# Kernel optimization log

Measured on AMD Instinct MI355X. Metric: run time of the kernel, lower is better.

The kernel has to match this reference:

```python
import jax, jax.numpy as jnp
import numpy as np

N = 100000   # nodes
R = 8        # relations
E = 800000   # edges per relation
D = 128      # in_feat == out_feat
B = 4        # num bases
L = 2        # ngnn layers


def setup_inputs() -> dict:
    key = jax.random.key(0)
    ks = jax.random.split(key, 8)
    x = jax.random.normal(ks[0], (N, D), dtype=jnp.float32)
    edge_src = jax.random.randint(ks[1], (R, E), 0, N, dtype=jnp.int64)
    edge_dst = jax.random.randint(ks[2], (R, E), 0, N, dtype=jnp.int64)
    scale = 1.0 / np.sqrt(D)
    w_comp = jax.random.normal(ks[3], (R, B), dtype=jnp.float32) * 0.3
    bases = jax.random.normal(ks[4], (B, D, D), dtype=jnp.float32) * scale
    loop_weight = jax.random.normal(ks[5], (D, D), dtype=jnp.float32) * scale
    h_bias = jnp.zeros((D,), dtype=jnp.float32)
    ngnn_w = jax.random.normal(ks[6], (L, D, D), dtype=jnp.float32) * scale
    return {"x": x, "edge_src": edge_src, "edge_dst": edge_dst,
            "w_comp": w_comp, "bases": bases, "loop_weight": loop_weight,
            "h_bias": h_bias, "ngnn_w": ngnn_w}


def reference(x, edge_src, edge_dst, w_comp, bases, loop_weight, h_bias, ngnn_w):
    # basis-decomposed per-relation weights: [R, D, D]
    weight = jnp.einsum('rb,bio->rio', w_comp, bases)
    h = jnp.zeros((N, D), dtype=x.dtype)
    # per-relation GraphConv, norm='right' (mean over in-degree, clamp min 1),
    # in_feat == out_feat so DGL aggregates first then applies weight;
    # HeteroGraphConv sums relation outputs for the shared dst type.
    for r in range(R):
        src, dst = edge_src[r], edge_dst[r]
        msg = jax.ops.segment_sum(x[src], dst, num_segments=N)           # [N, D]
        deg = jax.ops.segment_sum(jnp.ones((E,), x.dtype), dst, num_segments=N)
        agg = msg / jnp.maximum(deg, 1.0)[:, None]
        h = h + agg @ weight[r]
    # self loop + bias + activation
    h = jax.nn.relu(h + x @ loop_weight + h_bias)
    # NGNN MLP (dropout is identity in eval)
    for l in range(ngnn_w.shape[0]):
        h = jax.nn.relu(h @ ngnn_w[l])
    return h
```

## Files before the change

kernel.cpp:

```cpp
#include <hip/hip_runtime.h>
#include <hip/hip_bf16.h>

#define N_NODES 100000
#define R_REL   8
#define E_EDGES 800000
#define D_FEAT  128
#define B_BASES 4
#define RN      (R_REL * N_NODES)
#define RE      (R_REL * E_EDGES)

#define NBKT    784
#define BKT_CAP 9216
#define P1_TPB  256
#define P1_EPT  32
#define P1_CHUNK (P1_TPB * P1_EPT)
#define P1_NWG  ((RE + P1_CHUNK - 1) / P1_CHUNK)

#define SUB_PER_BKT 4
#define SGRID   (NBKT * SUB_PER_BKT)
#define SUBCAP  2816

typedef __attribute__((ext_vector_type(8))) short short8;
typedef __attribute__((ext_vector_type(4))) float floatx4;

__global__ __launch_bounds__(1024) void init_cursor_kernel(int* __restrict__ gcursor) {
    int t = threadIdx.x;
    if (t < NBKT) gcursor[t] = t * BKT_CAP;
}

__global__ __launch_bounds__(256) void xcvt_kernel(
    const float* __restrict__ x, uint* __restrict__ xb) {
    int i = blockIdx.x * 256 + threadIdx.x;
    if (i >= N_NODES * 64) return;
    float2 v = *(const float2*)(x + 2 * (size_t)i);
    __hip_bfloat162 h = __float22bfloat162_rn(v);
    xb[i] = *(uint*)&h;
}

__global__ __launch_bounds__(256) void wcvt_kernel(
    const float* __restrict__ bases, const float* __restrict__ loopw,
    unsigned short* __restrict__ wT) {
    int idx = blockIdx.x * 256 + threadIdx.x;
    if (idx >= 128 * 640) return;
    int n = idx / 640, k = idx % 640;
    float v = (k < 512) ? bases[(size_t)k * 128 + n] : loopw[(size_t)(k - 512) * 128 + n];
    __hip_bfloat16 h = __float2bfloat16(v);
    wT[idx] = *(unsigned short*)&h;
}

__global__ __launch_bounds__(256) void wcvt2_kernel(
    const float* __restrict__ ngnn_w, unsigned short* __restrict__ wT2) {
    int idx = blockIdx.x * 256 + threadIdx.x;
    if (idx >= 2 * 128 * 128) return;
    int l = idx >> 14, rem = idx & 16383;
    int n = rem >> 7, k = rem & 127;
    float v = ngnn_w[(size_t)l * 16384 + (size_t)k * 128 + n];
    __hip_bfloat16 h = __float2bfloat16(v);
    wT2[idx] = *(unsigned short*)&h;
}

__global__ __launch_bounds__(256) void p1_kernel(
    const int* __restrict__ src, const int* __restrict__ dst,
    int* __restrict__ gcursor, int* __restrict__ ebuf2) {
    __shared__ int hist[NBKT];
    __shared__ int cnt2[NBKT];
    __shared__ int basebkt[NBKT];
    __shared__ int lofs[NBKT];
    __shared__ int aux[256];
    __shared__ int recs[P1_CHUNK];
    __shared__ unsigned short bb[P1_CHUNK];
    int t = threadIdx.x;
    for (int i = t; i < NBKT; i += 256) { hist[i] = 0; cnt2[i] = 0; }
    __syncthreads();

    int e0 = blockIdx.x * P1_CHUNK;
    int rec[P1_EPT];
    int bkt[P1_EPT];
#pragma unroll
    for (int i = 0; i < P1_EPT; ++i) {
        int e = e0 + i * P1_TPB + t;
        if (e < RE) {
            int d = dst[e];
            int s = src[e];
            int r = e / E_EDGES;
            bkt[i] = d >> 7;
            rec[i] = s | ((d & 127) << 17) | (r << 24);
            atomicAdd(&hist[bkt[i]], 1);
        } else bkt[i] = -1;
    }
    __syncthreads();

    int k0 = t * 4;
    int c0 = (k0 + 0 < NBKT) ? hist[k0 + 0] : 0;
    int c1 = (k0 + 1 < NBKT) ? hist[k0 + 1] : 0;
    int c2 = (k0 + 2 < NBKT) ? hist[k0 + 2] : 0;
    int c3 = (k0 + 3 < NBKT) ? hist[k0 + 3] : 0;
    int s1 = c0 + c1, s2 = s1 + c2, s3 = s2 + c3;
    aux[t] = s3;
    __syncthreads();
    int vv = s3;
    for (int off = 1; off < 256; off <<= 1) {
        int yv = (t >= off) ? aux[t - off] : 0;
        __syncthreads();
        vv += yv;
        aux[t] = vv;
        __syncthreads();
    }
    int total = aux[255];
    int texcl = vv - s3;
    if (k0 + 0 < NBKT) lofs[k0 + 0] = texcl;
    if (k0 + 1 < NBKT) lofs[k0 + 1] = texcl + c0;
    if (k0 + 2 < NBKT) lofs[k0 + 2] = texcl + s1;
    if (k0 + 3 < NBKT) lofs[k0 + 3] = texcl + s2;
    __syncthreads();
    for (int i = t; i < NBKT; i += 256) {
        int hv = hist[i];
        basebkt[i] = (hv > 0) ? atomicAdd(&gcursor[i], hv) : 0;
    }
    __syncthreads();

#pragma unroll
    for (int i = 0; i < P1_EPT; ++i) {
        if (bkt[i] >= 0) {
            int p = lofs[bkt[i]] + atomicAdd(&cnt2[bkt[i]], 1);
            recs[p] = rec[i];
            bb[p] = (unsigned short)bkt[i];
        }
    }
    __syncthreads();

    for (int i = t; i < total; i += 256) {
        int b = bb[i];
        int p2 = basebkt[b] + (i - lofs[b]);
        if (p2 < (b + 1) * BKT_CAP) ebuf2[p2] = recs[i];
    }
}

template <bool XB>
__global__ __launch_bounds__(512, 8) void agg3_kernel(
    const float* __restrict__ x,
    const uint*  __restrict__ xb,
    const int*   __restrict__ gcursor,
    const int*   __restrict__ ebuf2,
    const float* __restrict__ w_comp,
    __hip_bfloat162* __restrict__ y) {
    __shared__ int raw[SUBCAP];
    __shared__ int sorted[SUBCAP];
    __shared__ int cursors[256];
    __shared__ int segbeg[256];
    __shared__ int nraw;
    const int t = threadIdx.x;
    const int bucket = blockIdx.x % NBKT;
    const int sub    = blockIdx.x / NBKT;

    int cnt = gcursor[bucket] - bucket * BKT_CAP;
    if (cnt > BKT_CAP) cnt = BKT_CAP;
    const int* brec = ebuf2 + (size_t)bucket * BKT_CAP;
    if (t < 256) cursors[t] = 0;
    if (t == 0) nraw = 0;
    __syncthreads();

    const int lane = t & 63;
    const unsigned long long lmask = (1ull << lane) - 1ull;

    for (int i0 = 0; i0 < cnt; i0 += 512) {
        int i = i0 + t;
        int rec = (i < cnt) ? brec[i] : 0;
        bool match = (i < cnt) && ((((rec >> 17) & 127) >> 5) == sub);
        unsigned long long mask = __ballot(match);
        int base = 0;
        if (lane == 0) base = atomicAdd(&nraw, (int)__popcll(mask));
        base = __shfl(base, 0);
        if (match) {
            int p = base + (int)__popcll(mask & lmask);
            if (p < SUBCAP) {
                raw[p] = rec;
                int key = ((rec >> 17) & 31) * 8 + ((rec >> 24) & 7);
                atomicAdd(&cursors[key], 1);
            }
        }
    }
    __syncthreads();
    int n = nraw; if (n > SUBCAP) n = SUBCAP;

    int deg = (t < 256) ? cursors[t] : 0;
    int* aux = sorted;
    aux[t] = deg;
    __syncthreads();
    int vv = deg;
    for (int off = 1; off < 256; off <<= 1) {
        int yv = (t >= off && t < 256) ? aux[t - off] : 0;
        __syncthreads();
        vv += yv;
        aux[t] = vv;
        __syncthreads();
    }
    if (t < 256) {
        cursors[t] = vv - deg;
        segbeg[t]  = vv - deg;
    }
    __syncthreads();

    for (int i = t; i < n; i += 512) {
        int rec = raw[i];
        int key = ((rec >> 17) & 31) * 8 + ((rec >> 24) & 7);
        int pos = atomicAdd(&cursors[key], 1);
        sorted[pos] = rec & 0x1FFFF;
    }
    __syncthreads();

    const int wid = t >> 6;
    const float* xp  = x + 2 * lane;
    const uint*  xbp = xb + lane;
    for (int nn = 0; nn < 4; ++nn) {
        int nl = wid * 4 + nn;
        int node = bucket * 128 + sub * 32 + nl;
        int key0 = nl * 8;
        float2 acc[B_BASES];
#pragma unroll
        for (int b = 0; b < B_BASES; ++b) acc[b] = make_float2(0.f, 0.f);
#pragma unroll
        for (int r = 0; r < R_REL; ++r) {
            int b0 = segbeg[key0 + r];
            int e0 = cursors[key0 + r];
            int d = e0 - b0;
            float inv = 1.0f / (float)(d > 1 ? d : 1);
            float ax = 0.f, ay = 0.f;
            int i = b0;
            for (; i + 3 < e0; i += 4) {
                int s0 = sorted[i], s1 = sorted[i + 1], s2 = sorted[i + 2], s3 = sorted[i + 3];
                if (XB) {
                    uint u0 = xbp[(size_t)s0 * 64];
                    uint u1 = xbp[(size_t)s1 * 64];
                    uint u2 = xbp[(size_t)s2 * 64];
                    uint u3 = xbp[(size_t)s3 * 64];
                    ax += (__uint_as_float(u0 << 16) + __uint_as_float(u1 << 16))
                        + (__uint_as_float(u2 << 16) + __uint_as_float(u3 << 16));
                    ay += (__uint_as_float(u0 & 0xFFFF0000u) + __uint_as_float(u1 & 0xFFFF0000u))
                        + (__uint_as_float(u2 & 0xFFFF0000u) + __uint_as_float(u3 & 0xFFFF0000u));
                } else {
                    float2 a = *(const float2*)(xp + (size_t)s0 * D_FEAT);
                    float2 b = *(const float2*)(xp + (size_t)s1 * D_FEAT);
                    float2 cc = *(const float2*)(xp + (size_t)s2 * D_FEAT);
                    float2 d2 = *(const float2*)(xp + (size_t)s3 * D_FEAT);
                    ax += (a.x + b.x) + (cc.x + d2.x);
                    ay += (a.y + b.y) + (cc.y + d2.y);
                }
            }
            for (; i < e0; ++i) {
                int s = sorted[i];
                if (XB) {
                    uint u = xbp[(size_t)s * 64];
                    ax += __uint_as_float(u << 16);
                    ay += __uint_as_float(u & 0xFFFF0000u);
                } else {
                    float2 a = *(const float2*)(xp + (size_t)s * D_FEAT);
                    ax += a.x; ay += a.y;
                }
            }
#pragma unroll
            for (int b = 0; b < B_BASES; ++b) {
                float coef = w_comp[r * B_BASES + b] * inv;
                acc[b].x = fmaf(coef, ax, acc[b].x);
                acc[b].y = fmaf(coef, ay, acc[b].y);
            }
        }
        if (node < N_NODES) {
#pragma unroll
            for (int b = 0; b < B_BASES; ++b)
                y[(size_t)node * 256 + b * 64 + lane] = __float22bfloat162_rn(acc[b]);
        }
    }
}

__global__ __launch_bounds__(256) void gemm_big_mfma(
    const short* __restrict__ y,
    const float* __restrict__ x,
    const unsigned short* __restrict__ wT,
    const float* __restrict__ bias,
    unsigned short* __restrict__ hb1) {
    const int wave = threadIdx.x >> 6;
    const int lane = threadIdx.x & 63;
    const int quad = lane >> 4;
    const int l16  = lane & 15;
    const int row0 = blockIdx.x * 64 + wave * 16;
    int arow = row0 + l16;
    if (arow >= N_NODES) arow = N_NODES - 1;

    floatx4 acc[8];
#pragma unroll
    for (int nt = 0; nt < 8; ++nt) acc[nt] = (floatx4){0.f, 0.f, 0.f, 0.f};

    const short* yrow = y + (size_t)arow * 512;
    const float* xrow = x + (size_t)arow * 128;
    const int koff = quad * 8;

    for (int ks = 0; ks < 16; ++ks) {
        int k0 = ks * 32 + koff;
        short8 a = *(const short8*)(yrow + k0);
#pragma unroll
        for (int nt = 0; nt < 8; ++nt) {
            int n = nt * 16 + l16;
            short8 b = *(const short8*)((const short*)wT + (size_t)n * 640 + k0);
            acc[nt] = __builtin_amdgcn_mfma_f32_16x16x32_bf16(a, b, acc[nt], 0, 0, 0);
        }
    }
#pragma unroll
    for (int ks = 0; ks < 4; ++ks) {
        int k0 = ks * 32 + koff;
        float4 fa = *(const float4*)(xrow + k0);
        float4 fb = *(const float4*)(xrow + k0 + 4);
        union { short8 s; uint u[4]; } ua;
        __hip_bfloat162 h0 = __float22bfloat162_rn(make_float2(fa.x, fa.y));
        __hip_bfloat162 h1 = __float22bfloat162_rn(make_float2(fa.z, fa.w));
        __hip_bfloat162 h2 = __float22bfloat162_rn(make_float2(fb.x, fb.y));
        __hip_bfloat162 h3 = __float22bfloat162_rn(make_float2(fb.z, fb.w));
        ua.u[0] = *(uint*)&h0; ua.u[1] = *(uint*)&h1;
        ua.u[2] = *(uint*)&h2; ua.u[3] = *(uint*)&h3;
#pragma unroll
        for (int nt = 0; nt < 8; ++nt) {
            int n = nt * 16 + l16;
            short8 b = *(const short8*)((const short*)wT + (size_t)n * 640 + 512 + k0);
            acc[nt] = __builtin_amdgcn_mfma_f32_16x16x32_bf16(ua.s, b, acc[nt], 0, 0, 0);
        }
    }

#pragma unroll
    for (int nt = 0; nt < 8; ++nt) {
        int n = nt * 16 + l16;
        float bs = bias[n];
#pragma unroll
        for (int i = 0; i < 4; ++i) {
            int m = row0 + quad * 4 + i;
            if (m < N_NODES) {
                float v = fmaxf(acc[nt][i] + bs, 0.f);
                __hip_bfloat16 h = __float2bfloat16(v);
                hb1[(size_t)m * D_FEAT + n] = *(unsigned short*)&h;
            }
        }
    }
}

template <bool OUT_BF16>
__global__ __launch_bounds__(256) void ngnn_mfma(
    const short* __restrict__ A,
    const unsigned short* __restrict__ wTl,
    void* __restrict__ C) {
    const int wave = threadIdx.x >> 6;
    const int lane = threadIdx.x & 63;
    const int quad = lane >> 4;
    const int l16  = lane & 15;
    const int row0 = blockIdx.x * 64 + wave * 16;
    int arow = row0 + l16;
    if (arow >= N_NODES) arow = N_NODES - 1;

    floatx4 acc[8];
#pragma unroll
    for (int nt = 0; nt < 8; ++nt) acc[nt] = (floatx4){0.f, 0.f, 0.f, 0.f};

    const short* ar = A + (size_t)arow * 128;
    const int koff = quad * 8;
#pragma unroll
    for (int ks = 0; ks < 4; ++ks) {
        int k0 = ks * 32 + koff;
        short8 a = *(const short8*)(ar + k0);
#pragma unroll
        for (int nt = 0; nt < 8; ++nt) {
            int n = nt * 16 + l16;
            short8 b = *(const short8*)((const short*)wTl + (size_t)n * 128 + k0);
            acc[nt] = __builtin_amdgcn_mfma_f32_16x16x32_bf16(a, b, acc[nt], 0, 0, 0);
        }
    }

#pragma unroll
    for (int nt = 0; nt < 8; ++nt) {
        int n = nt * 16 + l16;
#pragma unroll
        for (int i = 0; i < 4; ++i) {
            int m = row0 + quad * 4 + i;
            if (m < N_NODES) {
                float v = fmaxf(acc[nt][i], 0.f);
                if (OUT_BF16) {
                    __hip_bfloat16 h = __float2bfloat16(v);
                    ((unsigned short*)C)[(size_t)m * D_FEAT + n] = *(unsigned short*)&h;
                } else {
                    ((float*)C)[(size_t)m * D_FEAT + n] = v;
                }
            }
        }
    }
}

extern "C" void kernel_launch(void* const* d_in, const int* in_sizes, int n_in,
                              void* d_out, int out_size, void* d_ws, size_t ws_size,
                              hipStream_t stream) {
    const float* x           = (const float*)d_in[0];
    const int*   edge_src    = (const int*)d_in[1];
    const int*   edge_dst    = (const int*)d_in[2];
    const float* w_comp      = (const float*)d_in[3];
    const float* bases       = (const float*)d_in[4];
    const float* loop_weight = (const float*)d_in[5];
    const float* h_bias      = (const float*)d_in[6];
    const float* ngnn_w      = (const float*)d_in[7];
    float* out = (float*)d_out;

    char* ws = (char*)d_ws;
    size_t off = 0;
    __hip_bfloat162* y = (__hip_bfloat162*)(ws + off);
    off += (size_t)N_NODES * 512 * 2;
    int* ebuf2 = (int*)(ws + off);
    unsigned short* hb1 = (unsigned short*)(ws + off);
    off += (size_t)NBKT * BKT_CAP * 4;
    int* gcursor = (int*)(ws + off);
    off += 4096;
    unsigned short* wT = (unsigned short*)(ws + off);
    off += (size_t)128 * 640 * 2;
    unsigned short* wT2 = (unsigned short*)(ws + off);
    off += (size_t)2 * 128 * 128 * 2;
    uint* xb = (uint*)(ws + off);
    size_t xb_bytes = (size_t)N_NODES * 64 * 4;
    const bool use_bf16_x = (ws_size >= off + xb_bytes);
    unsigned short* hb2 = use_bf16_x ? (unsigned short*)xb : (unsigned short*)y;

    const int GEMM_GRID = (N_NODES + 63) / 64;

    wcvt_kernel<<<(128 * 640 + 255) / 256, 256, 0, stream>>>(bases, loop_weight, wT);
    wcvt2_kernel<<<(2 * 128 * 128 + 255) / 256, 256, 0, stream>>>(ngnn_w, wT2);
    if (use_bf16_x)
        xcvt_kernel<<<(N_NODES * 64 + 255) / 256, 256, 0, stream>>>(x, xb);

    init_cursor_kernel<<<1, 1024, 0, stream>>>(gcursor);
    p1_kernel<<<P1_NWG, P1_TPB, 0, stream>>>(edge_src, edge_dst, gcursor, ebuf2);

    if (use_bf16_x)
        agg3_kernel<true><<<SGRID, 512, 0, stream>>>(x, xb, gcursor, ebuf2, w_comp, y);
    else
        agg3_kernel<false><<<SGRID, 512, 0, stream>>>(x, nullptr, gcursor, ebuf2, w_comp, y);

    gemm_big_mfma<<<GEMM_GRID, 256, 0, stream>>>(
        (const short*)y, x, wT, h_bias, hb1);

    ngnn_mfma<true><<<GEMM_GRID, 256, 0, stream>>>(
        (const short*)hb1, wT2, (void*)hb2);
    ngnn_mfma<false><<<GEMM_GRID, 256, 0, stream>>>(
        (const short*)hb2, wT2 + 128 * 128, (void*)out);
}
```

Measured before the change: 701.2 us.

## Gather bf16 rows with 16-byte loads over four edges per wave

In the bf16 path of the aggregation kernel, each wave now splits into four 16-lane groups. Each group processes a different edge, and each lane loads a uint4 covering 8 features instead of one uint. Partial sums are combined with cross-lane shuffles before the bf16 store. The intent is fewer, wider gather instructions and more memory-level parallelism per wave, at the cost of more registers, extra shuffle reductions and masked tail handling. The block-to-bucket mapping also changes so that the four subblocks of a bucket are adjacent, and output stores become nontemporal.

```diff
diff --git a/kernel.cpp b/kernel.cpp
--- a/kernel.cpp
+++ b/kernel.cpp
@@ -135,6 +135,13 @@
         if (p2 < (b + 1) * BKT_CAP) ebuf2[p2] = recs[i];
     }
 }
+
+#define ACC4(u) do { \
+    ax0 += __uint_as_float((u).x << 16); ay0 += __uint_as_float((u).x & 0xFFFF0000u); \
+    ax1 += __uint_as_float((u).y << 16); ay1 += __uint_as_float((u).y & 0xFFFF0000u); \
+    ax2 += __uint_as_float((u).z << 16); ay2 += __uint_as_float((u).z & 0xFFFF0000u); \
+    ax3 += __uint_as_float((u).w << 16); ay3 += __uint_as_float((u).w & 0xFFFF0000u); \
+} while (0)
 
 template <bool XB>
 __global__ __launch_bounds__(512, 8) void agg3_kernel(
@@ -150,8 +157,8 @@
     __shared__ int segbeg[256];
     __shared__ int nraw;
     const int t = threadIdx.x;
-    const int bucket = blockIdx.x % NBKT;
-    const int sub    = blockIdx.x / NBKT;
+    const int bucket = blockIdx.x >> 2;
+    const int sub    = blockIdx.x & 3;
 
     int cnt = gcursor[bucket] - bucket * BKT_CAP;
     if (cnt > BKT_CAP) cnt = BKT_CAP;
@@ -210,35 +217,99 @@
     __syncthreads();
 
     const int wid = t >> 6;
-    const float* xp  = x + 2 * lane;
-    const uint*  xbp = xb + lane;
-    for (int nn = 0; nn < 4; ++nn) {
-        int nl = wid * 4 + nn;
-        int node = bucket * 128 + sub * 32 + nl;
-        int key0 = nl * 8;
-        float2 acc[B_BASES];
-#pragma unroll
-        for (int b = 0; b < B_BASES; ++b) acc[b] = make_float2(0.f, 0.f);
-#pragma unroll
-        for (int r = 0; r < R_REL; ++r) {
-            int b0 = segbeg[key0 + r];
-            int e0 = cursors[key0 + r];
-            int d = e0 - b0;
-            float inv = 1.0f / (float)(d > 1 ? d : 1);
-            float ax = 0.f, ay = 0.f;
-            int i = b0;
-            for (; i + 3 < e0; i += 4) {
-                int s0 = sorted[i], s1 = sorted[i + 1], s2 = sorted[i + 2], s3 = sorted[i + 3];
-                if (XB) {
-                    uint u0 = xbp[(size_t)s0 * 64];
-                    uint u1 = xbp[(size_t)s1 * 64];
-                    uint u2 = xbp[(size_t)s2 * 64];
-                    uint u3 = xbp[(size_t)s3 * 64];
-                    ax += (__uint_as_float(u0 << 16) + __uint_as_float(u1 << 16))
-                        + (__uint_as_float(u2 << 16) + __uint_as_float(u3 << 16));
-                    ay += (__uint_as_float(u0 & 0xFFFF0000u) + __uint_as_float(u1 & 0xFFFF0000u))
-                        + (__uint_as_float(u2 & 0xFFFF0000u) + __uint_as_float(u3 & 0xFFFF0000u));
-                } else {
+    if (XB) {
+        const int q  = lane & 15;
+        const int eg = lane >> 4;
+        const uint* xbq = xb + 4 * q;
+        for (int nn = 0; nn < 4; ++nn) {
+            int nl = wid * 4 + nn;
+            int node = bucket * 128 + sub * 32 + nl;
+            int key0 = nl * 8;
+            float2 a0[B_BASES], a1[B_BASES], a2[B_BASES], a3[B_BASES];
+#pragma unroll
+            for (int b = 0; b < B_BASES; ++b) {
+                a0[b] = make_float2(0.f, 0.f); a1[b] = make_float2(0.f, 0.f);
+                a2[b] = make_float2(0.f, 0.f); a3[b] = make_float2(0.f, 0.f);
+            }
+#pragma unroll
+            for (int r = 0; r < R_REL; ++r) {
+                int b0 = segbeg[key0 + r];
+                int e0 = cursors[key0 + r];
+                int len = e0 - b0;
+                float inv = 1.0f / (float)(len > 1 ? len : 1);
+                float ax0 = 0.f, ay0 = 0.f, ax1 = 0.f, ay1 = 0.f;
+                float ax2 = 0.f, ay2 = 0.f, ax3 = 0.f, ay3 = 0.f;
+                int it = 0;
+                for (; it + 8 <= len; it += 8) {
+                    int sA = sorted[b0 + it + eg];
+                    int sB = sorted[b0 + it + 4 + eg];
+                    uint4 uA = *(const uint4*)(xbq + (size_t)sA * 64);
+                    uint4 uB = *(const uint4*)(xbq + (size_t)sB * 64);
+                    ACC4(uA); ACC4(uB);
+                }
+                if (it + 4 <= len) {
+                    int sA = sorted[b0 + it + eg];
+                    uint4 uA = *(const uint4*)(xbq + (size_t)sA * 64);
+                    ACC4(uA);
+                    it += 4;
+                }
+                int rem = len - it;
+                if (rem > 0) {
+                    int idx = b0 + it + eg;
+                    int s = sorted[idx < e0 ? idx : e0 - 1];
+                    uint4 u = *(const uint4*)(xbq + (size_t)s * 64);
+                    if (eg >= rem) { u.x = 0u; u.y = 0u; u.z = 0u; u.w = 0u; }
+                    ACC4(u);
+                }
+#pragma unroll
+                for (int b = 0; b < B_BASES; ++b) {
+                    float c = w_comp[r * B_BASES + b] * inv;
+                    a0[b].x = fmaf(c, ax0, a0[b].x); a0[b].y = fmaf(c, ay0, a0[b].y);
+                    a1[b].x = fmaf(c, ax1, a1[b].x); a1[b].y = fmaf(c, ay1, a1[b].y);
+                    a2[b].x = fmaf(c, ax2, a2[b].x); a2[b].y = fmaf(c, ay2, a2[b].y);
+                    a3[b].x = fmaf(c, ax3, a3[b].x); a3[b].y = fmaf(c, ay3, a3[b].y);
+                }
+            }
+            if (node < N_NODES) {
+                uint* yrow = (uint*)(y + (size_t)node * 256);
+#pragma unroll
+                for (int b = 0; b < B_BASES; ++b) {
+                    float v0x = a0[b].x, v0y = a0[b].y, v1x = a1[b].x, v1y = a1[b].y;
+                    float v2x = a2[b].x, v2y = a2[b].y, v3x = a3[b].x, v3y = a3[b].y;
+                    v0x += __shfl_xor(v0x, 16); v0x += __shfl_xor(v0x, 32);
+                    v0y += __shfl_xor(v0y, 16); v0y += __shfl_xor(v0y, 32);
+                    v1x += __shfl_xor(v1x, 16); v1x += __shfl_xor(v1x, 32);
+                    v1y += __shfl_xor(v1y, 16); v1y += __shfl_xor(v1y, 32);
+                    v2x += __shfl_xor(v2x, 16); v2x += __shfl_xor(v2x, 32);
+                    v2y += __shfl_xor(v2y, 16); v2y += __shfl_xor(v2y, 32);
+                    v3x += __shfl_xor(v3x, 16); v3x += __shfl_xor(v3x, 32);
+                    v3y += __shfl_xor(v3y, 16); v3y += __shfl_xor(v3y, 32);
+                    float sx = (eg == 0) ? v0x : (eg == 1) ? v1x : (eg == 2) ? v2x : v3x;
+                    float sy = (eg == 0) ? v0y : (eg == 1) ? v1y : (eg == 2) ? v2y : v3y;
+                    __hip_bfloat162 h = __float22bfloat162_rn(make_float2(sx, sy));
+                    __builtin_nontemporal_store(*(uint*)&h, yrow + b * 64 + 4 * q + eg);
+                }
+            }
+        }
+    } else {
+        const float* xp = x + 2 * lane;
+        for (int nn = 0; nn < 4; ++nn) {
+            int nl = wid * 4 + nn;
+            int node = bucket * 128 + sub * 32 + nl;
+            int key0 = nl * 8;
+            float2 acc[B_BASES];
+#pragma unroll
+            for (int b = 0; b < B_BASES; ++b) acc[b] = make_float2(0.f, 0.f);
+#pragma unroll
+            for (int r = 0; r < R_REL; ++r) {
+                int b0 = segbeg[key0 + r];
+                int e0 = cursors[key0 + r];
+                int d = e0 - b0;
+                float inv = 1.0f / (float)(d > 1 ? d : 1);
+                float ax = 0.f, ay = 0.f;
+                int i = b0;
+                for (; i + 3 < e0; i += 4) {
+                    int s0 = sorted[i], s1 = sorted[i + 1], s2 = sorted[i + 2], s3 = sorted[i + 3];
                     float2 a = *(const float2*)(xp + (size_t)s0 * D_FEAT);
                     float2 b = *(const float2*)(xp + (size_t)s1 * D_FEAT);
                     float2 cc = *(const float2*)(xp + (size_t)s2 * D_FEAT);
@@ -246,29 +317,26 @@
                     ax += (a.x + b.x) + (cc.x + d2.x);
                     ay += (a.y + b.y) + (cc.y + d2.y);
                 }
-            }
-            for (; i < e0; ++i) {
-                int s = sorted[i];
-                if (XB) {
-                    uint u = xbp[(size_t)s * 64];
-                    ax += __uint_as_float(u << 16);
-                    ay += __uint_as_float(u & 0xFFFF0000u);
-                } else {
+                for (; i < e0; ++i) {
+                    int s = sorted[i];
                     float2 a = *(const float2*)(xp + (size_t)s * D_FEAT);
                     ax += a.x; ay += a.y;
                 }
-            }
-#pragma unroll
-            for (int b = 0; b < B_BASES; ++b) {
-                float coef = w_comp[r * B_BASES + b] * inv;
-                acc[b].x = fmaf(coef, ax, acc[b].x);
-                acc[b].y = fmaf(coef, ay, acc[b].y);
-            }
-        }
-        if (node < N_NODES) {
-#pragma unroll
-            for (int b = 0; b < B_BASES; ++b)
-                y[(size_t)node * 256 + b * 64 + lane] = __float22bfloat162_rn(acc[b]);
+#pragma unroll
+                for (int b = 0; b < B_BASES; ++b) {
+                    float coef = w_comp[r * B_BASES + b] * inv;
+                    acc[b].x = fmaf(coef, ax, acc[b].x);
+                    acc[b].y = fmaf(coef, ay, acc[b].y);
+                }
+            }
+            if (node < N_NODES) {
+                uint* yrow = (uint*)(y + (size_t)node * 256);
+#pragma unroll
+                for (int b = 0; b < B_BASES; ++b) {
+                    __hip_bfloat162 h = __float22bfloat162_rn(acc[b]);
+                    __builtin_nontemporal_store(*(uint*)&h, yrow + b * 64 + lane);
+                }
+            }
         }
     }
 }
```

Measured after the change: 1.614 ms. 2.3x slower.

## Fuse big GEMM and both NGNN layers into one kernel via LDS tiles

Applied to the files above, without the earlier changes.

Merges the main projection GEMM and the two NGNN MLP layers into one kernel. Each wave stages its 16x128 bf16 intermediate activations in a padded shared-memory tile instead of writing them to global memory. This removes two kernel launches and the global write and read of two N x 128 bf16 intermediates. In exchange it adds block-wide syncs and LDS traffic, and the fused kernel may use more registers.

```diff
diff --git a/kernel.cpp b/kernel.cpp
--- a/kernel.cpp
+++ b/kernel.cpp
@@ -273,12 +273,15 @@
     }
 }
 
-__global__ __launch_bounds__(256) void gemm_big_mfma(
+#define TPAD 136
+__global__ __launch_bounds__(256) void fused_mlp(
     const short* __restrict__ y,
     const float* __restrict__ x,
     const unsigned short* __restrict__ wT,
     const float* __restrict__ bias,
-    unsigned short* __restrict__ hb1) {
+    const unsigned short* __restrict__ wT2,
+    float* __restrict__ out) {
+    __shared__ short tile[4][16][TPAD];
     const int wave = threadIdx.x >> 6;
     const int lane = threadIdx.x & 63;
     const int quad = lane >> 4;
@@ -286,6 +289,7 @@
     const int row0 = blockIdx.x * 64 + wave * 16;
     int arow = row0 + l16;
     if (arow >= N_NODES) arow = N_NODES - 1;
+    short (*tl)[TPAD] = tile[wave];
 
     floatx4 acc[8];
 #pragma unroll
@@ -327,64 +331,56 @@
 
 #pragma unroll
     for (int nt = 0; nt < 8; ++nt) {
-        int n = nt * 16 + l16;
-        float bs = bias[n];
+        float bs = bias[nt * 16 + l16];
 #pragma unroll
         for (int i = 0; i < 4; ++i) {
-            int m = row0 + quad * 4 + i;
-            if (m < N_NODES) {
-                float v = fmaxf(acc[nt][i] + bs, 0.f);
-                __hip_bfloat16 h = __float2bfloat16(v);
-                hb1[(size_t)m * D_FEAT + n] = *(unsigned short*)&h;
-            }
-        }
-    }
-}
-
-template <bool OUT_BF16>
-__global__ __launch_bounds__(256) void ngnn_mfma(
-    const short* __restrict__ A,
-    const unsigned short* __restrict__ wTl,
-    void* __restrict__ C) {
-    const int wave = threadIdx.x >> 6;
-    const int lane = threadIdx.x & 63;
-    const int quad = lane >> 4;
-    const int l16  = lane & 15;
-    const int row0 = blockIdx.x * 64 + wave * 16;
-    int arow = row0 + l16;
-    if (arow >= N_NODES) arow = N_NODES - 1;
-
-    floatx4 acc[8];
-#pragma unroll
-    for (int nt = 0; nt < 8; ++nt) acc[nt] = (floatx4){0.f, 0.f, 0.f, 0.f};
-
-    const short* ar = A + (size_t)arow * 128;
-    const int koff = quad * 8;
-#pragma unroll
-    for (int ks = 0; ks < 4; ++ks) {
-        int k0 = ks * 32 + koff;
-        short8 a = *(const short8*)(ar + k0);
-#pragma unroll
-        for (int nt = 0; nt < 8; ++nt) {
-            int n = nt * 16 + l16;
-            short8 b = *(const short8*)((const short*)wTl + (size_t)n * 128 + k0);
-            acc[nt] = __builtin_amdgcn_mfma_f32_16x16x32_bf16(a, b, acc[nt], 0, 0, 0);
-        }
-    }
-
-#pragma unroll
-    for (int nt = 0; nt < 8; ++nt) {
-        int n = nt * 16 + l16;
-#pragma unroll
-        for (int i = 0; i < 4; ++i) {
-            int m = row0 + quad * 4 + i;
-            if (m < N_NODES) {
-                float v = fmaxf(acc[nt][i], 0.f);
-                if (OUT_BF16) {
+            float v = fmaxf(acc[nt][i] + bs, 0.f);
+            __hip_bfloat16 h = __float2bfloat16(v);
+            tl[quad * 4 + i][nt * 16 + l16] = *(short*)&h;
+        }
+    }
+    __syncthreads();
+
+#pragma unroll
+    for (int l = 0; l < 2; ++l) {
+        const unsigned short* wl = wT2 + l * 16384;
+        short8 af[4];
+#pragma unroll
+        for (int ks = 0; ks < 4; ++ks)
+            af[ks] = *(const short8*)&tl[l16][ks * 32 + koff];
+        floatx4 acc2[8];
+#pragma unroll
+        for (int nt = 0; nt < 8; ++nt) acc2[nt] = (floatx4){0.f, 0.f, 0.f, 0.f};
+#pragma unroll
+        for (int ks = 0; ks < 4; ++ks) {
+            int k0 = ks * 32 + koff;
+#pragma unroll
+            for (int nt = 0; nt < 8; ++nt) {
+                int n = nt * 16 + l16;
+                short8 b = *(const short8*)((const short*)wl + (size_t)n * 128 + k0);
+                acc2[nt] = __builtin_amdgcn_mfma_f32_16x16x32_bf16(af[ks], b, acc2[nt], 0, 0, 0);
+            }
+        }
+        if (l == 0) {
+            __syncthreads();
+#pragma unroll
+            for (int nt = 0; nt < 8; ++nt)
+#pragma unroll
+                for (int i = 0; i < 4; ++i) {
+                    float v = fmaxf(acc2[nt][i], 0.f);
                     __hip_bfloat16 h = __float2bfloat16(v);
-                    ((unsigned short*)C)[(size_t)m * D_FEAT + n] = *(unsigned short*)&h;
-                } else {
-                    ((float*)C)[(size_t)m * D_FEAT + n] = v;
+                    tl[quad * 4 + i][nt * 16 + l16] = *(short*)&h;
+                }
+            __syncthreads();
+        } else {
+#pragma unroll
+            for (int nt = 0; nt < 8; ++nt) {
+                int n = nt * 16 + l16;
+#pragma unroll
+                for (int i = 0; i < 4; ++i) {
+                    int m = row0 + quad * 4 + i;
+                    if (m < N_NODES)
+                        out[(size_t)m * D_FEAT + n] = fmaxf(acc2[nt][i], 0.f);
                 }
             }
         }
@@ -409,7 +405,6 @@
     __hip_bfloat162* y = (__hip_bfloat162*)(ws + off);
     off += (size_t)N_NODES * 512 * 2;
     int* ebuf2 = (int*)(ws + off);
-    unsigned short* hb1 = (unsigned short*)(ws + off);
     off += (size_t)NBKT * BKT_CAP * 4;
     int* gcursor = (int*)(ws + off);
     off += 4096;
@@ -420,7 +415,6 @@
     uint* xb = (uint*)(ws + off);
     size_t xb_bytes = (size_t)N_NODES * 64 * 4;
     const bool use_bf16_x = (ws_size >= off + xb_bytes);
-    unsigned short* hb2 = use_bf16_x ? (unsigned short*)xb : (unsigned short*)y;
 
     const int GEMM_GRID = (N_NODES + 63) / 64;
 
@@ -437,11 +431,6 @@
     else
         agg3_kernel<false><<<SGRID, 512, 0, stream>>>(x, nullptr, gcursor, ebuf2, w_comp, y);
 
-    gemm_big_mfma<<<GEMM_GRID, 256, 0, stream>>>(
-        (const short*)y, x, wT, h_bias, hb1);
-
-    ngnn_mfma<true><<<GEMM_GRID, 256, 0, stream>>>(
-        (const short*)hb1, wT2, (void*)hb2);
-    ngnn_mfma<false><<<GEMM_GRID, 256, 0, stream>>>(
-        (const short*)hb2, wT2 + 128 * 128, (void*)out);
-}
+    fused_mlp<<<GEMM_GRID, 256, 0, stream>>>(
+        (const short*)y, x, wT, h_bias, wT2, out);
+}
```

After: 675.4 us. -3.7%, faster.
